# Kernel tuning notes

Measured on AMD Instinct MI355X. Metric: run time of the kernel, lower is better.

Reference implementation:

```python
import jax, jax.numpy as jnp
import numpy as np

B, S, D, H = 8, 4096, 1024, 16
HD = D // H          # 64 head dim
NR = HD // 2         # 32 rotations
BASE = 10000.0


def setup_inputs() -> dict:
    key = jax.random.key(0)
    k0, k1, k2 = jax.random.split(key, 3)
    x = jax.random.normal(k0, (B, S, D), jnp.float32)
    thetas = jax.random.normal(k1, (NR,), jnp.float32) * 0.1
    r_pairs = jax.random.uniform(k2, (NR, 2), jnp.float32) * HD  # float indices in [0, HD)
    theta_scale = jnp.ones((1,), jnp.float32)
    n_rots_scale = jnp.ones((1,), jnp.float32)
    r_matrix = jnp.eye(HD, dtype=jnp.float32)
    inv_freq = 1.0 / (BASE ** (jnp.arange(0, HD, 2, dtype=jnp.float32) / HD))  # [HD/2]
    return {"x": x, "thetas": thetas, "r_pairs": r_pairs,
            "theta_scale": theta_scale, "n_rots_scale": n_rots_scale,
            "r_matrix": r_matrix, "inv_freq": inv_freq}


def reference(x, thetas, r_pairs, theta_scale, n_rots_scale, r_matrix, inv_freq):
    b, s, d = x.shape
    hd = r_matrix.shape[0]
    h = d // hd
    xf = x.reshape(-1, hd)  # [B*S*H, hd]

    # adjusted_n_rots = round(n_rots_scale * n_rots); n_rots_scale == 1 -> all rotations
    # (the int() in torch is non-differentiable/static anyway)
    idx = r_pairs.astype(jnp.int32)          # floor of non-negative floats, like .long()
    th = thetas * theta_scale[0]             # [NR]

    def step(xc, inp):
        i, j, t = inp
        c, sn = jnp.cos(t), jnp.sin(t)
        xi = xc[:, i]
        xj = xc[:, j]
        same = i == j
        # x @ G: col i -> xi*c + xj*s, col j -> -xi*s + xj*c; if i==j torch's
        # overwrite order leaves G[i,i] = cos -> col i = xi*c
        ni = jnp.where(same, xi * c, xi * c + xj * sn)
        nj = jnp.where(same, xi * c, -xi * sn + xj * c)
        xc = xc.at[:, i].set(ni)
        xc = xc.at[:, j].set(nj)
        return xc, None

    xf, _ = jax.lax.scan(step, xf, (idx[:, 0], idx[:, 1], th))
    xf = xf @ r_matrix                       # [B*S*H, hd]
    x4 = xf.reshape(b, s, h, hd)

    pos = jnp.arange(s, dtype=jnp.float32)
    sinusoid = pos[:, None] * inv_freq[None, :]        # [S, hd/2]
    sin = jnp.sin(sinusoid)[None, :, None, :]
    cos = jnp.cos(sinusoid)[None, :, None, :]
    x1 = x4[..., ::2]
    x2 = x4[..., 1::2]
    out = jnp.concatenate([x1 * cos - x2 * sin, x1 * sin + x2 * cos], axis=-1)
    return out.reshape(b, s, d)
```

## Files before the change

kernel.cpp:

```cpp
#include <hip/hip_runtime.h>

#define BB 8
#define SS 4096
#define DD 1024
#define HH 16
#define HD 64
#define NR 32
#define NROWS (BB * SS * HH)
#define NGRP (NROWS / 16)
#define GPW 4
#define GPB (4 * GPW)
#define NBLK (NGRP / GPB)

typedef __attribute__((ext_vector_type(8))) short bf16x8;
typedef __attribute__((ext_vector_type(4))) float f32x4;

__global__ __launch_bounds__(256) void build_pack_kernel(
    const float* __restrict__ thetas,
    const float* __restrict__ r_pairs,
    const float* __restrict__ theta_scale,
    const float* __restrict__ r_matrix,
    unsigned short* __restrict__ Apack)
{
    __shared__ float W[64 * 68];
    __shared__ int   ii[NR], jj[NR];
    __shared__ float cc[NR], ssn[NR];

    const int t = threadIdx.x;

#pragma unroll
    for (int it = 0; it < 16; ++it) {
        int idx = t + 256 * it;
        W[(idx >> 6) * 68 + (idx & 63)] = r_matrix[idx];
    }
    if (t < NR) {
        ii[t] = (int)r_pairs[2 * t];
        jj[t] = (int)r_pairs[2 * t + 1];
        float th = thetas[t] * theta_scale[0];
        cc[t]  = cosf(th);
        ssn[t] = sinf(th);
    }
    __syncthreads();

    if (t < 64) {
        for (int k = NR - 1; k >= 0; --k) {
            int i = ii[k], j = jj[k];
            float c = cc[k], s = ssn[k];
            float xi = W[i * 68 + t];
            float xj = W[j * 68 + t];
            if (i == j) {
                W[i * 68 + t] = c * xi;
            } else {
                W[i * 68 + t] = c * xi - s * xj;
                W[j * 68 + t] = s * xi + c * xj;
            }
        }
    }
    __syncthreads();

#pragma unroll
    for (int it = 0; it < 16; ++it) {
        int flat = t + 256 * it;
        int j    = flat & 7;
        int lane = (flat >> 3) & 63;
        int ks   = (flat >> 9) & 1;
        int tt   = flat >> 10;
        int i    = tt * 16 + (lane & 15);
        int k    = ks * 32 + ((lane >> 4) << 3) + j;
        float v  = W[k * 68 + i];
        unsigned u  = __float_as_uint(v);
        unsigned uh = u & 0xFFFF0000u;
        float fl    = v - __uint_as_float(uh);
        Apack[flat]        = (unsigned short)(uh >> 16);
        Apack[4096 + flat] = (unsigned short)(__float_as_uint(fl) >> 16);
    }
}

__device__ __forceinline__ void split8(const float4 a, const float4 b,
                                       bf16x8& hi, bf16x8& lo)
{
    const float f[8] = {a.x, a.y, a.z, a.w, b.x, b.y, b.z, b.w};
#pragma unroll
    for (int j = 0; j < 8; ++j) {
        unsigned u  = __float_as_uint(f[j]);
        unsigned uh = u & 0xFFFF0000u;
        hi[j] = (short)(uh >> 16);
        float fl = f[j] - __uint_as_float(uh);
        lo[j] = (short)(__float_as_uint(fl) >> 16);
    }
}

__global__ __launch_bounds__(256, 4) void rope_mfma_kernel(
    const float* __restrict__ x,
    const unsigned short* __restrict__ Apack,
    const float* __restrict__ inv_freq,
    float* __restrict__ out)
{
    const int lane = threadIdx.x & 63;
    const int wv   = threadIdx.x >> 6;
    const int q    = lane >> 4;
    const int rr   = lane & 15;
    const int qlo  = q & 1;
    const int qhi  = q >> 1;
    const bool odd = qlo != 0;

    bf16x8 Ah[4][2], Al[4][2];
    {
        const bf16x8* Ap = (const bf16x8*)Apack;
#pragma unroll
        for (int tt = 0; tt < 4; ++tt)
#pragma unroll
            for (int ks = 0; ks < 2; ++ks) {
                Ah[tt][ks] = Ap[(tt * 2 + ks) * 64 + lane];
                Al[tt][ks] = Ap[512 + (tt * 2 + ks) * 64 + lane];
            }
    }
    float4 invf4[2];
#pragma unroll
    for (int pr = 0; pr < 2; ++pr)
        invf4[pr] = *(const float4*)&inv_freq[8 * qlo + 4 * qhi + 16 * pr];

    int g = blockIdx.x * GPB + wv * GPW;

    const float* xr = x + ((size_t)g * 16 + rr) * 64 + q * 8;
    float4 fa0 = *(const float4*)(xr);
    float4 fa1 = *(const float4*)(xr + 4);
    float4 fa2 = *(const float4*)(xr + 32);
    float4 fa3 = *(const float4*)(xr + 36);

#pragma unroll 1
    for (int gi = 0; gi < GPW; ++gi, ++g) {
        float4 fb0 = fa0, fb1 = fa1, fb2 = fa2, fb3 = fa3;
        if (gi + 1 < GPW) {
            const float* xn = x + ((size_t)(g + 1) * 16 + rr) * 64 + q * 8;
            fb0 = *(const float4*)(xn);
            fb1 = *(const float4*)(xn + 4);
            fb2 = *(const float4*)(xn + 32);
            fb3 = *(const float4*)(xn + 36);
        }

        bf16x8 Bh0, Bl0, Bh1, Bl1;
        split8(fa0, fa1, Bh0, Bl0);
        split8(fa2, fa3, Bh1, Bl1);

        f32x4 acc[4];
#pragma unroll
        for (int tt = 0; tt < 4; ++tt) {
            f32x4 a = {0.f, 0.f, 0.f, 0.f};
            a = __builtin_amdgcn_mfma_f32_16x16x32_bf16(Ah[tt][0], Bh0, a, 0, 0, 0);
            a = __builtin_amdgcn_mfma_f32_16x16x32_bf16(Ah[tt][1], Bh1, a, 0, 0, 0);
            a = __builtin_amdgcn_mfma_f32_16x16x32_bf16(Al[tt][0], Bh0, a, 0, 0, 0);
            a = __builtin_amdgcn_mfma_f32_16x16x32_bf16(Al[tt][1], Bh1, a, 0, 0, 0);
            a = __builtin_amdgcn_mfma_f32_16x16x32_bf16(Ah[tt][0], Bl0, a, 0, 0, 0);
            a = __builtin_amdgcn_mfma_f32_16x16x32_bf16(Ah[tt][1], Bl1, a, 0, 0, 0);
            acc[tt] = a;
        }

        const float pos = (float)(g & (SS - 1));
        float* orow = out + ((size_t)g * 16 + rr) * 64;

#pragma unroll
        for (int pr = 0; pr < 2; ++pr) {
            const f32x4 aE = acc[2 * pr];
            const f32x4 aO = acc[2 * pr + 1];
            float y8[8];
#pragma unroll
            for (int r = 0; r < 4; ++r) {
                float send = odd ? aE[r] : aO[r];
                float recv = __shfl_xor(send, 16, 64);
                y8[r]     = odd ? recv  : aE[r];
                y8[4 + r] = odd ? aO[r] : recv;
            }
            const float4 fr = invf4[pr];
            float sn[4], cs[4];
            __sincosf(pos * fr.x, &sn[0], &cs[0]);
            __sincosf(pos * fr.y, &sn[1], &cs[1]);
            __sincosf(pos * fr.z, &sn[2], &cs[2]);
            __sincosf(pos * fr.w, &sn[3], &cs[3]);
            f32x4 o1, o2;
            o1[0] = y8[0] * cs[0] - y8[1] * sn[0];
            o1[1] = y8[2] * cs[1] - y8[3] * sn[1];
            o1[2] = y8[4] * cs[2] - y8[5] * sn[2];
            o1[3] = y8[6] * cs[3] - y8[7] * sn[3];
            o2[0] = y8[0] * sn[0] + y8[1] * cs[0];
            o2[1] = y8[2] * sn[1] + y8[3] * cs[1];
            o2[2] = y8[4] * sn[2] + y8[5] * cs[2];
            o2[3] = y8[6] * sn[3] + y8[7] * cs[3];
            const int cb4 = 8 * qlo + 4 * qhi + 16 * pr;
            __builtin_nontemporal_store(o1, (f32x4*)(orow + cb4));
            __builtin_nontemporal_store(o2, (f32x4*)(orow + 32 + cb4));
        }

        fa0 = fb0; fa1 = fb1; fa2 = fb2; fa3 = fb3;
    }
}

extern "C" void kernel_launch(void* const* d_in, const int* in_sizes, int n_in,
                              void* d_out, int out_size, void* d_ws, size_t ws_size,
                              hipStream_t stream)
{
    const float* x           = (const float*)d_in[0];
    const float* thetas      = (const float*)d_in[1];
    const float* r_pairs     = (const float*)d_in[2];
    const float* theta_scale = (const float*)d_in[3];
    const float* r_matrix    = (const float*)d_in[5];
    const float* inv_freq    = (const float*)d_in[6];
    float* out = (float*)d_out;
    unsigned short* Apack = (unsigned short*)d_ws;

    build_pack_kernel<<<1, 256, 0, stream>>>(thetas, r_pairs, theta_scale,
                                             r_matrix, Apack);
    rope_mfma_kernel<<<NBLK, 256, 0, stream>>>(x, Apack, inv_freq, out);
}
```

Before: 264.3 us.

## Stage packed rotation matrix in LDS and process two row groups per wave

Each block now copies the packed bf16 hi/lo rotation matrix into shared memory once, and waves read A fragments from LDS instead of keeping 64 VGPRs of them per lane. Each wave handles two groups with fully unrolled straight-line code. Both groups' x loads are issued up front and their MFMA chains are interleaved so the two accumulators hide each other's latency. Stores switch from nontemporal to plain, and the block count doubles. This adds a per-block 16KB global-to-LDS copy, a barrier, and LDS read traffic in exchange for fewer registers and more memory-level parallelism.

```diff
diff --git a/kernel.cpp b/kernel.cpp
--- a/kernel.cpp
+++ b/kernel.cpp
@@ -8,7 +8,7 @@
 #define NR 32
 #define NROWS (BB * SS * HH)
 #define NGRP (NROWS / 16)
-#define GPW 4
+#define GPW 2
 #define GPB (4 * GPW)
 #define NBLK (NGRP / GPB)
 
@@ -90,109 +90,127 @@
     }
 }
 
+__device__ __forceinline__ void epilogue(
+    int g, const f32x4 acc[4], int rr, bool odd, int qlo, int qhi,
+    const float4 invf4[2], float* __restrict__ out)
+{
+    const float pos = (float)(g & (SS - 1));
+    float* orow = out + ((size_t)g * 16 + rr) * 64;
+#pragma unroll
+    for (int pr = 0; pr < 2; ++pr) {
+        const f32x4 aE = acc[2 * pr];
+        const f32x4 aO = acc[2 * pr + 1];
+        float y8[8];
+#pragma unroll
+        for (int r = 0; r < 4; ++r) {
+            float send = odd ? aE[r] : aO[r];
+            float recv = __shfl_xor(send, 16, 64);
+            y8[r]     = odd ? recv  : aE[r];
+            y8[4 + r] = odd ? aO[r] : recv;
+        }
+        const float4 fr = invf4[pr];
+        float sn[4], cs[4];
+        __sincosf(pos * fr.x, &sn[0], &cs[0]);
+        __sincosf(pos * fr.y, &sn[1], &cs[1]);
+        __sincosf(pos * fr.z, &sn[2], &cs[2]);
+        __sincosf(pos * fr.w, &sn[3], &cs[3]);
+        f32x4 o1, o2;
+        o1[0] = y8[0] * cs[0] - y8[1] * sn[0];
+        o1[1] = y8[2] * cs[1] - y8[3] * sn[1];
+        o1[2] = y8[4] * cs[2] - y8[5] * sn[2];
+        o1[3] = y8[6] * cs[3] - y8[7] * sn[3];
+        o2[0] = y8[0] * sn[0] + y8[1] * cs[0];
+        o2[1] = y8[2] * sn[1] + y8[3] * cs[1];
+        o2[2] = y8[4] * sn[2] + y8[5] * cs[2];
+        o2[3] = y8[6] * sn[3] + y8[7] * cs[3];
+        const int cb4 = 8 * qlo + 4 * qhi + 16 * pr;
+        *(f32x4*)(orow + cb4)      = o1;
+        *(f32x4*)(orow + 32 + cb4) = o2;
+    }
+}
+
 __global__ __launch_bounds__(256, 4) void rope_mfma_kernel(
     const float* __restrict__ x,
     const unsigned short* __restrict__ Apack,
     const float* __restrict__ inv_freq,
     float* __restrict__ out)
 {
-    const int lane = threadIdx.x & 63;
-    const int wv   = threadIdx.x >> 6;
+    __shared__ unsigned short Asm[8192];
+
+    const int t = threadIdx.x;
+
+    {
+        const f32x4* src = (const f32x4*)Apack;
+        f32x4*       dst = (f32x4*)Asm;
+#pragma unroll
+        for (int it = 0; it < 4; ++it)
+            dst[t + 256 * it] = src[t + 256 * it];
+    }
+    __syncthreads();
+
+    const int lane = t & 63;
+    const int wv   = t >> 6;
     const int q    = lane >> 4;
     const int rr   = lane & 15;
     const int qlo  = q & 1;
     const int qhi  = q >> 1;
     const bool odd = qlo != 0;
 
-    bf16x8 Ah[4][2], Al[4][2];
-    {
-        const bf16x8* Ap = (const bf16x8*)Apack;
-#pragma unroll
-        for (int tt = 0; tt < 4; ++tt)
-#pragma unroll
-            for (int ks = 0; ks < 2; ++ks) {
-                Ah[tt][ks] = Ap[(tt * 2 + ks) * 64 + lane];
-                Al[tt][ks] = Ap[512 + (tt * 2 + ks) * 64 + lane];
-            }
-    }
     float4 invf4[2];
 #pragma unroll
     for (int pr = 0; pr < 2; ++pr)
         invf4[pr] = *(const float4*)&inv_freq[8 * qlo + 4 * qhi + 16 * pr];
 
-    int g = blockIdx.x * GPB + wv * GPW;
-
-    const float* xr = x + ((size_t)g * 16 + rr) * 64 + q * 8;
-    float4 fa0 = *(const float4*)(xr);
-    float4 fa1 = *(const float4*)(xr + 4);
-    float4 fa2 = *(const float4*)(xr + 32);
-    float4 fa3 = *(const float4*)(xr + 36);
-
-#pragma unroll 1
-    for (int gi = 0; gi < GPW; ++gi, ++g) {
-        float4 fb0 = fa0, fb1 = fa1, fb2 = fa2, fb3 = fa3;
-        if (gi + 1 < GPW) {
-            const float* xn = x + ((size_t)(g + 1) * 16 + rr) * 64 + q * 8;
-            fb0 = *(const float4*)(xn);
-            fb1 = *(const float4*)(xn + 4);
-            fb2 = *(const float4*)(xn + 32);
-            fb3 = *(const float4*)(xn + 36);
-        }
-
-        bf16x8 Bh0, Bl0, Bh1, Bl1;
-        split8(fa0, fa1, Bh0, Bl0);
-        split8(fa2, fa3, Bh1, Bl1);
-
-        f32x4 acc[4];
-#pragma unroll
-        for (int tt = 0; tt < 4; ++tt) {
-            f32x4 a = {0.f, 0.f, 0.f, 0.f};
-            a = __builtin_amdgcn_mfma_f32_16x16x32_bf16(Ah[tt][0], Bh0, a, 0, 0, 0);
-            a = __builtin_amdgcn_mfma_f32_16x16x32_bf16(Ah[tt][1], Bh1, a, 0, 0, 0);
-            a = __builtin_amdgcn_mfma_f32_16x16x32_bf16(Al[tt][0], Bh0, a, 0, 0, 0);
-            a = __builtin_amdgcn_mfma_f32_16x16x32_bf16(Al[tt][1], Bh1, a, 0, 0, 0);
-            a = __builtin_amdgcn_mfma_f32_16x16x32_bf16(Ah[tt][0], Bl0, a, 0, 0, 0);
-            a = __builtin_amdgcn_mfma_f32_16x16x32_bf16(Ah[tt][1], Bl1, a, 0, 0, 0);
-            acc[tt] = a;
-        }
-
-        const float pos = (float)(g & (SS - 1));
-        float* orow = out + ((size_t)g * 16 + rr) * 64;
-
-#pragma unroll
-        for (int pr = 0; pr < 2; ++pr) {
-            const f32x4 aE = acc[2 * pr];
-            const f32x4 aO = acc[2 * pr + 1];
-            float y8[8];
-#pragma unroll
-            for (int r = 0; r < 4; ++r) {
-                float send = odd ? aE[r] : aO[r];
-                float recv = __shfl_xor(send, 16, 64);
-                y8[r]     = odd ? recv  : aE[r];
-                y8[4 + r] = odd ? aO[r] : recv;
-            }
-            const float4 fr = invf4[pr];
-            float sn[4], cs[4];
-            __sincosf(pos * fr.x, &sn[0], &cs[0]);
-            __sincosf(pos * fr.y, &sn[1], &cs[1]);
-            __sincosf(pos * fr.z, &sn[2], &cs[2]);
-            __sincosf(pos * fr.w, &sn[3], &cs[3]);
-            f32x4 o1, o2;
-            o1[0] = y8[0] * cs[0] - y8[1] * sn[0];
-            o1[1] = y8[2] * cs[1] - y8[3] * sn[1];
-            o1[2] = y8[4] * cs[2] - y8[5] * sn[2];
-            o1[3] = y8[6] * cs[3] - y8[7] * sn[3];
-            o2[0] = y8[0] * sn[0] + y8[1] * cs[0];
-            o2[1] = y8[2] * sn[1] + y8[3] * cs[1];
-            o2[2] = y8[4] * sn[2] + y8[5] * cs[2];
-            o2[3] = y8[6] * sn[3] + y8[7] * cs[3];
-            const int cb4 = 8 * qlo + 4 * qhi + 16 * pr;
-            __builtin_nontemporal_store(o1, (f32x4*)(orow + cb4));
-            __builtin_nontemporal_store(o2, (f32x4*)(orow + 32 + cb4));
-        }
-
-        fa0 = fb0; fa1 = fb1; fa2 = fb2; fa3 = fb3;
-    }
+    const int g0 = blockIdx.x * GPB + wv * GPW;
+
+    const float* xr0 = x + ((size_t)g0 * 16 + rr) * 64 + q * 8;
+    const float4 f00 = *(const float4*)(xr0);
+    const float4 f01 = *(const float4*)(xr0 + 4);
+    const float4 f02 = *(const float4*)(xr0 + 32);
+    const float4 f03 = *(const float4*)(xr0 + 36);
+    const float* xr1 = xr0 + 1024;
+    const float4 f10 = *(const float4*)(xr1);
+    const float4 f11 = *(const float4*)(xr1 + 4);
+    const float4 f12 = *(const float4*)(xr1 + 32);
+    const float4 f13 = *(const float4*)(xr1 + 36);
+
+    bf16x8 B0h0, B0l0, B0h1, B0l1;
+    bf16x8 B1h0, B1l0, B1h1, B1l1;
+    split8(f00, f01, B0h0, B0l0);
+    split8(f02, f03, B0h1, B0l1);
+    split8(f10, f11, B1h0, B1l0);
+    split8(f12, f13, B1h1, B1l1);
+
+    const bf16x8* Ap = (const bf16x8*)Asm;
+
+    f32x4 acc0[4], acc1[4];
+#pragma unroll
+    for (int tt = 0; tt < 4; ++tt) {
+        const bf16x8 ah0 = Ap[(tt * 2 + 0) * 64 + lane];
+        const bf16x8 ah1 = Ap[(tt * 2 + 1) * 64 + lane];
+        const bf16x8 al0 = Ap[512 + (tt * 2 + 0) * 64 + lane];
+        const bf16x8 al1 = Ap[512 + (tt * 2 + 1) * 64 + lane];
+
+        f32x4 a = {0.f, 0.f, 0.f, 0.f};
+        f32x4 b = {0.f, 0.f, 0.f, 0.f};
+        a = __builtin_amdgcn_mfma_f32_16x16x32_bf16(ah0, B0h0, a, 0, 0, 0);
+        b = __builtin_amdgcn_mfma_f32_16x16x32_bf16(ah0, B1h0, b, 0, 0, 0);
+        a = __builtin_amdgcn_mfma_f32_16x16x32_bf16(ah1, B0h1, a, 0, 0, 0);
+        b = __builtin_amdgcn_mfma_f32_16x16x32_bf16(ah1, B1h1, b, 0, 0, 0);
+        a = __builtin_amdgcn_mfma_f32_16x16x32_bf16(al0, B0h0, a, 0, 0, 0);
+        b = __builtin_amdgcn_mfma_f32_16x16x32_bf16(al0, B1h0, b, 0, 0, 0);
+        a = __builtin_amdgcn_mfma_f32_16x16x32_bf16(al1, B0h1, a, 0, 0, 0);
+        b = __builtin_amdgcn_mfma_f32_16x16x32_bf16(al1, B1h1, b, 0, 0, 0);
+        a = __builtin_amdgcn_mfma_f32_16x16x32_bf16(ah0, B0l0, a, 0, 0, 0);
+        b = __builtin_amdgcn_mfma_f32_16x16x32_bf16(ah0, B1l0, b, 0, 0, 0);
+        a = __builtin_amdgcn_mfma_f32_16x16x32_bf16(ah1, B0l1, a, 0, 0, 0);
+        b = __builtin_amdgcn_mfma_f32_16x16x32_bf16(ah1, B1l1, b, 0, 0, 0);
+        acc0[tt] = a;
+        acc1[tt] = b;
+    }
+
+    epilogue(g0,     acc0, rr, odd, qlo, qhi, invf4, out);
+    epilogue(g0 + 1, acc1, rr, odd, qlo, qhi, invf4, out);
 }
 
 extern "C" void kernel_launch(void* const* d_in, const int* in_sizes, int n_in,
```

New measurement: 246.2 us. 1.07x faster.
